# Optimization experiments

Measured on AMD Instinct MI355X. Metric: run time of the kernel, lower is better.

Reference implementation:

```python
import jax, jax.numpy as jnp
import numpy as np

B, S, H = 2, 2048, 1024
HFF = 4096
E, K = 8, 2

def setup_inputs() -> dict:
    key = jax.random.key(0)
    k1, k2, k3, k4, k5 = jax.random.split(key, 5)
    x = jax.random.normal(k1, (B, S, H), dtype=jnp.float32)
    topk_probs = jax.random.uniform(k2, (B, S, K), dtype=jnp.float32)
    topk_indices = jax.random.randint(k3, (B, S, K), 0, E, dtype=jnp.int64)
    stdv = 1.0 / np.sqrt(H)
    W1 = jax.random.uniform(k4, (E, HFF, H), minval=-stdv, maxval=stdv, dtype=jnp.float32)
    stdv2 = 1.0 / np.sqrt(HFF)
    W2 = jax.random.uniform(k5, (E, H, HFF), minval=-stdv2, maxval=stdv2, dtype=jnp.float32)
    return {"x": x, "topk_probs": topk_probs, "topk_indices": topk_indices, "W1": W1, "W2": W2}

def reference(x, topk_probs, topk_indices, W1, W2):
    # gate[b,s,e] = max_k topk_probs[b,s,k] * (topk_indices[b,s,k]==e)
    # (max over k, matching probs_mask.max(dim=-1) in the torch module)
    e_ids = jnp.arange(E, dtype=topk_indices.dtype)  # [E]
    sel = topk_indices[..., None] == e_ids  # [B,S,K,E]
    gate = jnp.max(jnp.where(sel, topk_probs[..., None], 0.0), axis=2)  # [B,S,E]
    # dense per-expert FFN over all tokens (as the original computes)
    h = jnp.einsum('bsh,efh->ebsf', x, W1)       # [E,B,S,HFF]
    h = jax.nn.gelu(h)
    y = jnp.einsum('ebsf,ehf->ebsh', h, W2)      # [E,B,S,H]
    # probability applied after FFN, masked combine over experts
    out = jnp.einsum('bse,ebsh->bsh', gate, y)   # [B,S,H]
    return out
```

## Files before the change

kernel.cpp:

```cpp
#include <hip/hip_runtime.h>

typedef unsigned short ushort_t;
typedef __attribute__((ext_vector_type(8))) short short8;
typedef __attribute__((ext_vector_type(4))) float f32x4;

#define TOKENS  4096
#define H_DIM   1024
#define HFF_DIM 4096
#define NEXP    8

#define XCVT_BLOCKS  (TOKENS * H_DIM / 8 / 256)
#define W1CVT_BLOCKS (NEXP * HFF_DIM * H_DIM / 8 / 256)
#define W2CVT_BLOCKS (NEXP * H_DIM * HFF_DIM / 8 / 256)
#define G1_BLOCKS    (NEXP * 32 * 32)
#define G2_BLOCKS    (NEXP * 32 * 8)

__device__ __forceinline__ ushort_t f2b(float f) {
    union { float f; unsigned u; } v; v.f = f;
    unsigned r = v.u + 0x7fffu + ((v.u >> 16) & 1u);
    return (ushort_t)(r >> 16);
}

__device__ __forceinline__ void cvt8(const float* __restrict__ src,
                                     ushort_t* __restrict__ dst, size_t i) {
    const float4* s = (const float4*)(src + i * 8);
    float4 a = s[0], b = s[1];
    ushort_t o[8];
    o[0] = f2b(a.x); o[1] = f2b(a.y); o[2] = f2b(a.z); o[3] = f2b(a.w);
    o[4] = f2b(b.x); o[5] = f2b(b.y); o[6] = f2b(b.z); o[7] = f2b(b.w);
    *(short8*)(dst + i * 8) = *(short8*)o;
}

__device__ __forceinline__ float gelu_tanh(float x) {
    float u = 0.7978845608028654f * (x + 0.044715f * x * x * x);
    return 0.5f * x * (1.0f + tanhf(u));
}

__device__ __forceinline__ void gload16(const ushort_t* g, ushort_t* l) {
    __builtin_amdgcn_global_load_lds(
        (const __attribute__((address_space(1))) unsigned int*)g,
        (__attribute__((address_space(3))) unsigned int*)l,
        16, 0, 0);
}

__global__ void prep_kernel(const float* __restrict__ probs,
                            const int* __restrict__ idx,
                            const float* __restrict__ x,
                            ushort_t* __restrict__ xb,
                            const float* __restrict__ W1,
                            ushort_t* __restrict__ W1b,
                            int* __restrict__ count,
                            int* __restrict__ token_id,
                            float* __restrict__ gate) {
    const int wg = blockIdx.x;
    if (wg >= XCVT_BLOCKS) {
        cvt8(W1, W1b, (size_t)(wg - XCVT_BLOCKS) * 256 + threadIdx.x);
        return;
    }
    const int gid = wg * 256 + threadIdx.x;
    cvt8(x, xb, (size_t)gid);

    if (wg >= TOKENS / 256) return;
    const int t = gid;
    const int lane = threadIdx.x & 63;

    const int i0 = idx[t * 2 + 0];
    const int i1 = idx[t * 2 + 1];
    const float p0 = probs[t * 2 + 0];
    const float p1 = probs[t * 2 + 1];
    const bool dup = (i0 == i1);
    const float q0 = dup ? fmaxf(p0, p1) : p0;

#pragma unroll
    for (int k = 0; k < 2; ++k) {
        const int want = (k == 0) ? i0 : (dup ? -1 : i1);
        const float p  = (k == 0) ? q0 : p1;
#pragma unroll
        for (int e = 0; e < NEXP; ++e) {
            unsigned long long m = __ballot(want == e);
            if (m == 0ull) continue;
            if (want == e) {
                const int lead = __ffsll((long long)m) - 1;
                int base = 0;
                if (lane == lead) base = atomicAdd(&count[e], (int)__popcll(m));
                base = __shfl(base, lead);
                const int pos = base + (int)__popcll(m & ((1ull << lane) - 1ull));
                token_id[e * TOKENS + pos] = t;
                gate[e * TOKENS + pos] = p;
            }
        }
    }
}

__global__ void cvt_kernel(const float* __restrict__ src, ushort_t* __restrict__ dst, int n8) {
    int i = blockIdx.x * blockDim.x + threadIdx.x;
    if (i >= n8) return;
    cvt8(src, dst, (size_t)i);
}

__global__ __launch_bounds__(256) void gemm1_kernel(
        const ushort_t* __restrict__ xb, const ushort_t* __restrict__ W1b,
        const int* __restrict__ count, const int* __restrict__ token_id,
        ushort_t* __restrict__ h,
        const float* __restrict__ W2, ushort_t* __restrict__ W2b) {
    if (blockIdx.x >= G1_BLOCKS) {
        cvt8(W2, W2b, (size_t)(blockIdx.x - G1_BLOCKS) * 256 + threadIdx.x);
        return;
    }
    const int wg  = blockIdx.x;
    const int swz = (wg & 7) * (G1_BLOCKS / 8) + (wg >> 3);
    const int e   = swz >> 10;
    const int rem = swz & 1023;
    const int mt  = rem >> 5;
    const int nt  = rem & 31;

    const int cnt = count[e];
    if (mt * 128 >= cnt) return;
    int base = 0;
    for (int i = 0; i < e; ++i) base += count[i];

    __shared__ __align__(16) ushort_t As[128 * 32];
    __shared__ __align__(16) ushort_t Bs[128 * 32];

    const int tid = threadIdx.x;
    const int lane = tid & 63;
    const int wave = tid >> 6;

    const int sr0 = (wave << 5) + (lane >> 2);
    const int sr1 = sr0 + 16;
    const int sc  = (lane & 3) << 3;

    int ra0 = mt * 128 + sr0; if (ra0 >= cnt) ra0 = cnt - 1;
    int ra1 = mt * 128 + sr1; if (ra1 >= cnt) ra1 = cnt - 1;
    const int t0 = token_id[e * TOKENS + ra0];
    const int t1 = token_id[e * TOKENS + ra1];
    const ushort_t* pa0 = xb + (size_t)t0 * H_DIM + sc;
    const ushort_t* pa1 = xb + (size_t)t1 * H_DIM + sc;
    const ushort_t* pb0 = W1b + (size_t)e * HFF_DIM * H_DIM
                          + (size_t)(nt * 128 + sr0) * H_DIM + sc;
    const ushort_t* pb1 = pb0 + (size_t)16 * H_DIM;
    ushort_t* lA0 = &As[wave << 10];
    ushort_t* lA1 = lA0 + 512;
    ushort_t* lB0 = &Bs[wave << 10];
    ushort_t* lB1 = lB0 + 512;

    const int wm = (wave >> 1) << 6;
    const int wn = (wave & 1) << 6;
    const int lr = lane & 15;
    const int lq = lane >> 4;

    f32x4 acc[4][4];
#pragma unroll
    for (int mi = 0; mi < 4; ++mi)
#pragma unroll
        for (int ni = 0; ni < 4; ++ni)
            acc[mi][ni] = (f32x4){0.f, 0.f, 0.f, 0.f};

    for (int k0 = 0; k0 < H_DIM; k0 += 32) {
        __syncthreads();
        gload16(pa0 + k0, lA0);
        gload16(pa1 + k0, lA1);
        gload16(pb0 + k0, lB0);
        gload16(pb1 + k0, lB1);
        __syncthreads();

        short8 af[4], bf[4];
#pragma unroll
        for (int mi = 0; mi < 4; ++mi)
            af[mi] = *(const short8*)&As[(wm + mi * 16 + lr) * 32 + lq * 8];
#pragma unroll
        for (int ni = 0; ni < 4; ++ni)
            bf[ni] = *(const short8*)&Bs[(wn + ni * 16 + lr) * 32 + lq * 8];
#pragma unroll
        for (int mi = 0; mi < 4; ++mi)
#pragma unroll
            for (int ni = 0; ni < 4; ++ni)
                acc[mi][ni] = __builtin_amdgcn_mfma_f32_16x16x32_bf16(
                    af[mi], bf[ni], acc[mi][ni], 0, 0, 0);
    }

#pragma unroll
    for (int mi = 0; mi < 4; ++mi) {
#pragma unroll
        for (int r = 0; r < 4; ++r) {
            int m = mt * 128 + wm + mi * 16 + lq * 4 + r;
            if (m < cnt) {
                ushort_t* hp = h + (size_t)(base + m) * HFF_DIM + nt * 128 + wn + lr;
#pragma unroll
                for (int ni = 0; ni < 4; ++ni)
                    hp[ni * 16] = f2b(gelu_tanh(acc[mi][ni][r]));
            }
        }
    }
}

__global__ __launch_bounds__(256) void gemm2_kernel(
        const ushort_t* __restrict__ h, const ushort_t* __restrict__ W2b,
        const int* __restrict__ count, const int* __restrict__ token_id,
        const float* __restrict__ gate, float* __restrict__ out) {
    const int wg  = blockIdx.x;
    const int swz = (wg & 7) * (G2_BLOCKS / 8) + (wg >> 3);
    const int e   = swz >> 8;
    const int rem = swz & 255;
    const int mt  = rem >> 3;
    const int nt  = rem & 7;

    const int cnt = count[e];
    if (mt * 128 >= cnt) return;
    int base = 0;
    for (int i = 0; i < e; ++i) base += count[i];

    __shared__ __align__(16) ushort_t As[128 * 32];
    __shared__ __align__(16) ushort_t Bs[128 * 32];

    const int tid = threadIdx.x;
    const int lane = tid & 63;
    const int wave = tid >> 6;

    const int sr0 = (wave << 5) + (lane >> 2);
    const int sr1 = sr0 + 16;
    const int sc  = (lane & 3) << 3;

    int ra0 = mt * 128 + sr0; if (ra0 >= cnt) ra0 = cnt - 1;
    int ra1 = mt * 128 + sr1; if (ra1 >= cnt) ra1 = cnt - 1;
    const ushort_t* pa0 = h + (size_t)(base + ra0) * HFF_DIM + sc;
    const ushort_t* pa1 = h + (size_t)(base + ra1) * HFF_DIM + sc;
    const ushort_t* pb0 = W2b + (size_t)e * H_DIM * HFF_DIM
                          + (size_t)(nt * 128 + sr0) * HFF_DIM + sc;
    const ushort_t* pb1 = pb0 + (size_t)16 * HFF_DIM;
    ushort_t* lA0 = &As[wave << 10];
    ushort_t* lA1 = lA0 + 512;
    ushort_t* lB0 = &Bs[wave << 10];
    ushort_t* lB1 = lB0 + 512;

    const int wm = (wave >> 1) << 6;
    const int wn = (wave & 1) << 6;
    const int lr = lane & 15;
    const int lq = lane >> 4;

    f32x4 acc[4][4];
#pragma unroll
    for (int mi = 0; mi < 4; ++mi)
#pragma unroll
        for (int ni = 0; ni < 4; ++ni)
            acc[mi][ni] = (f32x4){0.f, 0.f, 0.f, 0.f};

    for (int k0 = 0; k0 < HFF_DIM; k0 += 32) {
        __syncthreads();
        gload16(pa0 + k0, lA0);
        gload16(pa1 + k0, lA1);
        gload16(pb0 + k0, lB0);
        gload16(pb1 + k0, lB1);
        __syncthreads();

        short8 af[4], bf[4];
#pragma unroll
        for (int mi = 0; mi < 4; ++mi)
            af[mi] = *(const short8*)&As[(wm + mi * 16 + lr) * 32 + lq * 8];
#pragma unroll
        for (int ni = 0; ni < 4; ++ni)
            bf[ni] = *(const short8*)&Bs[(wn + ni * 16 + lr) * 32 + lq * 8];
#pragma unroll
        for (int mi = 0; mi < 4; ++mi)
#pragma unroll
            for (int ni = 0; ni < 4; ++ni)
                acc[mi][ni] = __builtin_amdgcn_mfma_f32_16x16x32_bf16(
                    af[mi], bf[ni], acc[mi][ni], 0, 0, 0);
    }

#pragma unroll
    for (int mi = 0; mi < 4; ++mi) {
#pragma unroll
        for (int r = 0; r < 4; ++r) {
            int m = mt * 128 + wm + mi * 16 + lq * 4 + r;
            if (m < cnt) {
                int tok = token_id[e * TOKENS + m];
                float g = gate[e * TOKENS + m];
                float* op = out + (size_t)tok * H_DIM + nt * 128 + wn + lr;
#pragma unroll
                for (int ni = 0; ni < 4; ++ni)
                    atomicAdd(&op[ni * 16], g * acc[mi][ni][r]);
            }
        }
    }
}

extern "C" void kernel_launch(void* const* d_in, const int* in_sizes, int n_in,
                              void* d_out, int out_size, void* d_ws, size_t ws_size,
                              hipStream_t stream) {
    const float* x     = (const float*)d_in[0];
    const float* probs = (const float*)d_in[1];
    const int*   idx   = (const int*)d_in[2];
    const float* W1    = (const float*)d_in[3];
    const float* W2    = (const float*)d_in[4];
    float* out = (float*)d_out;

    char* ws = (char*)d_ws;
    int*      count    = (int*)ws;
    int*      token_id = (int*)(ws + 4096);
    float*    gate     = (float*)(ws + 4096 + 8 * TOKENS * 4);
    ushort_t* xb       = (ushort_t*)(ws + ((size_t)1 << 20));
    ushort_t* W1b      = (ushort_t*)(ws + ((size_t)9 << 20));

    const bool overlap = ws_size >= ((size_t)201 << 20);
    ushort_t* W2b = overlap ? (ushort_t*)(ws + ((size_t)73 << 20)) : W1b;
    ushort_t* h   = overlap ? (ushort_t*)(ws + ((size_t)137 << 20))
                            : (ushort_t*)(ws + ((size_t)73 << 20));

    hipMemsetAsync(count, 0, 64, stream);
    hipMemsetAsync(out, 0, (size_t)out_size * sizeof(float), stream);

    prep_kernel<<<XCVT_BLOCKS + W1CVT_BLOCKS, 256, 0, stream>>>(
        probs, idx, x, xb, W1, W1b, count, token_id, gate);

    if (overlap) {
        gemm1_kernel<<<G1_BLOCKS + W2CVT_BLOCKS, 256, 0, stream>>>(
            xb, W1b, count, token_id, h, W2, W2b);
    } else {
        gemm1_kernel<<<G1_BLOCKS, 256, 0, stream>>>(
            xb, W1b, count, token_id, h, W2, W2b);
        int n8 = NEXP * H_DIM * HFF_DIM / 8;
        cvt_kernel<<<(n8 + 255) / 256, 256, 0, stream>>>(W2, W2b, n8);
    }

    gemm2_kernel<<<G2_BLOCKS, 256, 0, stream>>>(h, W2b, count, token_id, gate, out);
}
```

Baseline: 535.2 us.

## Shrink expert GEMM tiles to 64x128 with two-wave workgroups

Both grouped GEMMs move from a 128x128 tile with four waves to a 64x128 tile with two waves, each wave computing 64x64. The load assignment is reworked so wave 0 fetches the gathered A rows plus part of B while wave 1 fetches the rest of B. The goal is less padding waste on partial expert M-tiles and more workgroups for better occupancy. The cost is that B traffic per output roughly doubles, the loads are unevenly split between the two waves, and the W2 conversion block count is adjusted to match the 128-thread launch.

New measurement: 560.9 us. 1.05x slower.

```diff
diff --git a/kernel.cpp b/kernel.cpp
--- a/kernel.cpp
+++ b/kernel.cpp
@@ -11,9 +11,9 @@
 
 #define XCVT_BLOCKS  (TOKENS * H_DIM / 8 / 256)
 #define W1CVT_BLOCKS (NEXP * HFF_DIM * H_DIM / 8 / 256)
-#define W2CVT_BLOCKS (NEXP * H_DIM * HFF_DIM / 8 / 256)
-#define G1_BLOCKS    (NEXP * 32 * 32)
-#define G2_BLOCKS    (NEXP * 32 * 8)
+#define W2CVT_BLOCKS (NEXP * H_DIM * HFF_DIM / 8 / 128)
+#define G1_BLOCKS    (NEXP * 64 * 32)
+#define G2_BLOCKS    (NEXP * 64 * 8)
 
 __device__ __forceinline__ ushort_t f2b(float f) {
     union { float f; unsigned u; } v; v.f = f;
@@ -98,54 +98,64 @@
     cvt8(src, dst, (size_t)i);
 }
 
-__global__ __launch_bounds__(256) void gemm1_kernel(
+
+__global__ __launch_bounds__(128) void gemm1_kernel(
         const ushort_t* __restrict__ xb, const ushort_t* __restrict__ W1b,
         const int* __restrict__ count, const int* __restrict__ token_id,
         ushort_t* __restrict__ h,
         const float* __restrict__ W2, ushort_t* __restrict__ W2b) {
     if (blockIdx.x >= G1_BLOCKS) {
-        cvt8(W2, W2b, (size_t)(blockIdx.x - G1_BLOCKS) * 256 + threadIdx.x);
+        cvt8(W2, W2b, (size_t)(blockIdx.x - G1_BLOCKS) * 128 + threadIdx.x);
         return;
     }
     const int wg  = blockIdx.x;
     const int swz = (wg & 7) * (G1_BLOCKS / 8) + (wg >> 3);
-    const int e   = swz >> 10;
-    const int rem = swz & 1023;
+    const int e   = swz >> 11;
+    const int rem = swz & 2047;
     const int mt  = rem >> 5;
     const int nt  = rem & 31;
 
     const int cnt = count[e];
-    if (mt * 128 >= cnt) return;
+    if (mt * 64 >= cnt) return;
     int base = 0;
     for (int i = 0; i < e; ++i) base += count[i];
 
-    __shared__ __align__(16) ushort_t As[128 * 32];
+    __shared__ __align__(16) ushort_t As[64 * 32];
     __shared__ __align__(16) ushort_t Bs[128 * 32];
 
     const int tid = threadIdx.x;
     const int lane = tid & 63;
     const int wave = tid >> 6;
 
-    const int sr0 = (wave << 5) + (lane >> 2);
-    const int sr1 = sr0 + 16;
+    const int r16 = lane >> 2;
     const int sc  = (lane & 3) << 3;
 
-    int ra0 = mt * 128 + sr0; if (ra0 >= cnt) ra0 = cnt - 1;
-    int ra1 = mt * 128 + sr1; if (ra1 >= cnt) ra1 = cnt - 1;
-    const int t0 = token_id[e * TOKENS + ra0];
-    const int t1 = token_id[e * TOKENS + ra1];
-    const ushort_t* pa0 = xb + (size_t)t0 * H_DIM + sc;
-    const ushort_t* pa1 = xb + (size_t)t1 * H_DIM + sc;
-    const ushort_t* pb0 = W1b + (size_t)e * HFF_DIM * H_DIM
-                          + (size_t)(nt * 128 + sr0) * H_DIM + sc;
-    const ushort_t* pb1 = pb0 + (size_t)16 * H_DIM;
-    ushort_t* lA0 = &As[wave << 10];
-    ushort_t* lA1 = lA0 + 512;
-    ushort_t* lB0 = &Bs[wave << 10];
-    ushort_t* lB1 = lB0 + 512;
-
-    const int wm = (wave >> 1) << 6;
-    const int wn = (wave & 1) << 6;
+    const ushort_t* sp[6];
+    ushort_t* ld[6];
+    const ushort_t* Wbase = W1b + (size_t)e * HFF_DIM * H_DIM;
+    if (wave == 0) {
+#pragma unroll
+        for (int g = 0; g < 4; ++g) {
+            int ra = mt * 64 + g * 16 + r16;
+            if (ra >= cnt) ra = cnt - 1;
+            const int tok = token_id[e * TOKENS + ra];
+            sp[g] = xb + (size_t)tok * H_DIM + sc;
+            ld[g] = &As[g * 512];
+        }
+#pragma unroll
+        for (int g = 0; g < 2; ++g) {
+            sp[4 + g] = Wbase + (size_t)(nt * 128 + g * 16 + r16) * H_DIM + sc;
+            ld[4 + g] = &Bs[g * 512];
+        }
+    } else {
+#pragma unroll
+        for (int g = 0; g < 6; ++g) {
+            sp[g] = Wbase + (size_t)(nt * 128 + (g + 2) * 16 + r16) * H_DIM + sc;
+            ld[g] = &Bs[(g + 2) * 512];
+        }
+    }
+
+    const int wn = wave << 6;
     const int lr = lane & 15;
     const int lq = lane >> 4;
 
@@ -158,16 +168,15 @@
 
     for (int k0 = 0; k0 < H_DIM; k0 += 32) {
         __syncthreads();
-        gload16(pa0 + k0, lA0);
-        gload16(pa1 + k0, lA1);
-        gload16(pb0 + k0, lB0);
-        gload16(pb1 + k0, lB1);
+#pragma unroll
+        for (int g = 0; g < 6; ++g)
+            gload16(sp[g] + k0, ld[g]);
         __syncthreads();
 
         short8 af[4], bf[4];
 #pragma unroll
         for (int mi = 0; mi < 4; ++mi)
-            af[mi] = *(const short8*)&As[(wm + mi * 16 + lr) * 32 + lq * 8];
+            af[mi] = *(const short8*)&As[(mi * 16 + lr) * 32 + lq * 8];
 #pragma unroll
         for (int ni = 0; ni < 4; ++ni)
             bf[ni] = *(const short8*)&Bs[(wn + ni * 16 + lr) * 32 + lq * 8];
@@ -183,7 +192,7 @@
     for (int mi = 0; mi < 4; ++mi) {
 #pragma unroll
         for (int r = 0; r < 4; ++r) {
-            int m = mt * 128 + wm + mi * 16 + lq * 4 + r;
+            int m = mt * 64 + mi * 16 + lq * 4 + r;
             if (m < cnt) {
                 ushort_t* hp = h + (size_t)(base + m) * HFF_DIM + nt * 128 + wn + lr;
 #pragma unroll
@@ -194,47 +203,57 @@
     }
 }
 
-__global__ __launch_bounds__(256) void gemm2_kernel(
+__global__ __launch_bounds__(128) void gemm2_kernel(
         const ushort_t* __restrict__ h, const ushort_t* __restrict__ W2b,
         const int* __restrict__ count, const int* __restrict__ token_id,
         const float* __restrict__ gate, float* __restrict__ out) {
     const int wg  = blockIdx.x;
     const int swz = (wg & 7) * (G2_BLOCKS / 8) + (wg >> 3);
-    const int e   = swz >> 8;
-    const int rem = swz & 255;
+    const int e   = swz >> 9;
+    const int rem = swz & 511;
     const int mt  = rem >> 3;
     const int nt  = rem & 7;
 
     const int cnt = count[e];
-    if (mt * 128 >= cnt) return;
+    if (mt * 64 >= cnt) return;
     int base = 0;
     for (int i = 0; i < e; ++i) base += count[i];
 
-    __shared__ __align__(16) ushort_t As[128 * 32];
+    __shared__ __align__(16) ushort_t As[64 * 32];
     __shared__ __align__(16) ushort_t Bs[128 * 32];
 
     const int tid = threadIdx.x;
     const int lane = tid & 63;
     const int wave = tid >> 6;
 
-    const int sr0 = (wave << 5) + (lane >> 2);
-    const int sr1 = sr0 + 16;
+    const int r16 = lane >> 2;
     const int sc  = (lane & 3) << 3;
 
-    int ra0 = mt * 128 + sr0; if (ra0 >= cnt) ra0 = cnt - 1;
-    int ra1 = mt * 128 + sr1; if (ra1 >= cnt) ra1 = cnt - 1;
-    const ushort_t* pa0 = h + (size_t)(base + ra0) * HFF_DIM + sc;
-    const ushort_t* pa1 = h + (size_t)(base + ra1) * HFF_DIM + sc;
-    const ushort_t* pb0 = W2b + (size_t)e * H_DIM * HFF_DIM
-                          + (size_t)(nt * 128 + sr0) * HFF_DIM + sc;
-    const ushort_t* pb1 = pb0 + (size_t)16 * HFF_DIM;
-    ushort_t* lA0 = &As[wave << 10];
-    ushort_t* lA1 = lA0 + 512;
-    ushort_t* lB0 = &Bs[wave << 10];
-    ushort_t* lB1 = lB0 + 512;
-
-    const int wm = (wave >> 1) << 6;
-    const int wn = (wave & 1) << 6;
+    const ushort_t* sp[6];
+    ushort_t* ld[6];
+    const ushort_t* Wbase = W2b + (size_t)e * H_DIM * HFF_DIM;
+    if (wave == 0) {
+#pragma unroll
+        for (int g = 0; g < 4; ++g) {
+            int ra = mt * 64 + g * 16 + r16;
+            if (ra >= cnt) ra = cnt - 1;
+            sp[g] = h + (size_t)(base + ra) * HFF_DIM + sc;
+            ld[g] = &As[g * 512];
+        }
+#pragma unroll
+        for (int g = 0; g < 2; ++g) {
+            sp[4 + g] = Wbase + (size_t)(nt * 128 + g * 16 + r16) * HFF_DIM + sc;
+            ld[4 + g] = &Bs[g * 512];
+        }
+    } else {
+#pragma unroll
+        for (int g = 0; g < 6; ++g) {
+            sp[g] = Wbase + (size_t)(nt * 128 + (g + 2) * 16 + r16) * HFF_DIM + sc;
+            ld[g] = &Bs[(g + 2) * 512];
+        }
+    }
+
+    const int wn = wave << 6;
     const int lr = lane & 15;
     const int lq = lane >> 4;
 
@@ -247,16 +266,15 @@
 
     for (int k0 = 0; k0 < HFF_DIM; k0 += 32) {
         __syncthreads();
-        gload16(pa0 + k0, lA0);
-        gload16(pa1 + k0, lA1);
-        gload16(pb0 + k0, lB0);
-        gload16(pb1 + k0, lB1);
+#pragma unroll
+        for (int g = 0; g < 6; ++g)
+            gload16(sp[g] + k0, ld[g]);
         __syncthreads();
 
         short8 af[4], bf[4];
 #pragma unroll
         for (int mi = 0; mi < 4; ++mi)
-            af[mi] = *(const short8*)&As[(wm + mi * 16 + lr) * 32 + lq * 8];
+            af[mi] = *(const short8*)&As[(mi * 16 + lr) * 32 + lq * 8];
 #pragma unroll
         for (int ni = 0; ni < 4; ++ni)
             bf[ni] = *(const short8*)&Bs[(wn + ni * 16 + lr) * 32 + lq * 8];
@@ -272,7 +290,7 @@
     for (int mi = 0; mi < 4; ++mi) {
 #pragma unroll
         for (int r = 0; r < 4; ++r) {
-            int m = mt * 128 + wm + mi * 16 + lq * 4 + r;
+            int m = mt * 64 + mi * 16 + lq * 4 + r;
             if (m < cnt) {
                 int tok = token_id[e * TOKENS + m];
                 float g = gate[e * TOKENS + m];
@@ -314,14 +332,14 @@
         probs, idx, x, xb, W1, W1b, count, token_id, gate);
 
     if (overlap) {
-        gemm1_kernel<<<G1_BLOCKS + W2CVT_BLOCKS, 256, 0, stream>>>(
+        gemm1_kernel<<<G1_BLOCKS + W2CVT_BLOCKS, 128, 0, stream>>>(
             xb, W1b, count, token_id, h, W2, W2b);
     } else {
-        gemm1_kernel<<<G1_BLOCKS, 256, 0, stream>>>(
+        gemm1_kernel<<<G1_BLOCKS, 128, 0, stream>>>(
             xb, W1b, count, token_id, h, W2, W2b);
         int n8 = NEXP * H_DIM * HFF_DIM / 8;
         cvt_kernel<<<(n8 + 255) / 256, 256, 0, stream>>>(W2, W2b, n8);
     }
 
-    gemm2_kernel<<<G2_BLOCKS, 256, 0, stream>>>(h, W2b, count, token_id, gate, out);
-}
+    gemm2_kernel<<<G2_BLOCKS, 128, 0, stream>>>(h, W2b, count, token_id, gate, out);
+}
```
